# Kernel optimization log

Measured on AMD Instinct MI355X. Metric: run time of the kernel, lower is better.

The kernel has to match this reference:

```python
import jax, jax.numpy as jnp
import numpy as np
import math

B, N, D, H = 2, 64, 256, 8
DK = D // H


def setup_inputs() -> dict:
    key = jax.random.key(0)
    ks = jax.random.split(key, 12)
    s = 1.0 / math.sqrt(D)
    inp = {
        "state": jax.random.normal(ks[0], (B, N, N, D), dtype=jnp.float32),
        "mask": jnp.zeros((B, N, N, N), dtype=bool),
        "W_lk": jax.random.normal(ks[1], (D, D), dtype=jnp.float32) * s,
        "b_lk": jnp.zeros((D,), dtype=jnp.float32),
        "W_rk": jax.random.normal(ks[2], (D, D), dtype=jnp.float32) * s,
        "b_rk": jnp.zeros((D,), dtype=jnp.float32),
        "W_lv": jax.random.normal(ks[3], (D, D), dtype=jnp.float32) * s,
        "b_lv": jnp.zeros((D,), dtype=jnp.float32),
        "W_rv": jax.random.normal(ks[4], (D, D), dtype=jnp.float32) * s,
        "b_rv": jnp.zeros((D,), dtype=jnp.float32),
        "W_o": jax.random.normal(ks[5], (D, D), dtype=jnp.float32) * s,
        "b_o": jnp.zeros((D,), dtype=jnp.float32),
    }
    return inp


def _proj(x, W, b):
    # torch nn.Linear: x @ W.T + b, then view to heads
    y = jnp.einsum('bxyd,ed->bxye', x, W) + b
    return y.reshape(B, N, N, H, DK)


def reference(state, mask, W_lk, b_lk, W_rk, b_rk, W_lv, b_lv, W_rv, b_rv, W_o, b_o):
    left_k = _proj(state, W_lk, b_lk)   # [B,N,N,H,DK]
    right_k = _proj(state, W_rk, b_rk)
    left_v = _proj(state, W_lv, b_lv)
    right_v = _proj(state, W_rv, b_rv)

    # triangle-style scores over node triples (x, a, y): [B,N,N,N,H]
    scores = jnp.einsum('bxahd,bayhd->bxayh', left_k, right_k) / math.sqrt(DK)
    scores = jnp.where(mask[..., None], jnp.float32(-1000.0), scores)
    att = jax.nn.softmax(scores, axis=2)  # softmax over intermediate node a

    # val[b,x,a,y,h,d] = left_v[b,x,a,h,d] * right_v[b,a,y,h,d] (materialized as in torch)
    val = jnp.einsum('bxahd,bayhd->bxayhd', left_v, right_v)
    x = jnp.einsum('bxayh,bxayhd->bxyhd', att, val)  # sum over a
    x = x.reshape(B, N, N, D)
    return jnp.einsum('bxyd,ed->bxye', x, W_o) + b_o
```

## Files before the change

kernel.cpp:

```cpp
#include <hip/hip_runtime.h>

#define B 2
#define N 64
#define D 256
#define H 8
#define DK 32
#define M (B * N * N)

typedef __attribute__((ext_vector_type(8))) short bf16x8;
typedef __attribute__((ext_vector_type(4))) float f32x4;
typedef __attribute__((ext_vector_type(2))) float f32x2;

#define PROJ_ELEMS (2097152)

__device__ __forceinline__ ushort f2b(float f) {
    union { float f; unsigned u; } v; v.f = f;
    unsigned r = v.u + 0x7fffu + ((v.u >> 16) & 1u);
    return (ushort)(r >> 16);
}
__device__ __forceinline__ float b2f(ushort u) {
    union { unsigned u; float f; } v; v.u = ((unsigned)u) << 16; return v.f;
}
__device__ __forceinline__ f32x2 up2(unsigned u) {
    union { unsigned u; float f; } lo, hi;
    lo.u = u << 16; hi.u = u & 0xffff0000u;
    f32x2 r; r.x = lo.f; r.y = hi.f; return r;
}

__device__ __forceinline__ void glds16(const ushort* g, ushort* l) {
    __builtin_amdgcn_global_load_lds(
        (const __attribute__((address_space(1))) unsigned int*)g,
        (__attribute__((address_space(3))) unsigned int*)l, 16, 0, 0);
}

__global__ __launch_bounds__(256) void cast_all(const float* __restrict__ state,
                                                const float* __restrict__ W_lk, const float* __restrict__ W_rk,
                                                const float* __restrict__ W_lv, const float* __restrict__ W_rv,
                                                const float* __restrict__ W_o,
                                                const float* __restrict__ b_lk, const float* __restrict__ b_rk,
                                                const float* __restrict__ b_lv, const float* __restrict__ b_rv,
                                                const float* __restrict__ b_o,
                                                ushort* __restrict__ state_bf,
                                                ushort* __restrict__ Wcat,
                                                float* __restrict__ bias_cat) {
    const int gid = blockIdx.x * 256 + threadIdx.x;
    const float* Ws[5] = {W_lk, W_rk, W_lv, W_rv, W_o};
    const float* bs[5] = {b_lk, b_rk, b_lv, b_rv, b_o};

    if (gid < 1280) bias_cat[gid] = bs[gid >> 8][gid & 255];

    if (gid < 524288) {
        float4 v = *(const float4*)&state[(size_t)gid * 4];
        ushort4 o = {f2b(v.x), f2b(v.y), f2b(v.z), f2b(v.w)};
        *(ushort4*)&state_bf[(size_t)gid * 4] = o;
    } else {
        int u = gid - 524288;
        int row = u >> 6;
        int k4 = (u & 63) * 4;
        const float* W = Ws[row >> 8];
        float4 v = *(const float4*)&W[(size_t)(row & 255) * 256 + k4];
        ushort4 o = {f2b(v.x), f2b(v.y), f2b(v.z), f2b(v.w)};
        *(ushort4*)&Wcat[(size_t)row * 256 + k4] = o;
    }
}

template <int BF16OUT, int RELAYOUT>
__global__ __launch_bounds__(256) void gemm_mfma(const ushort* __restrict__ A,
                                                 const ushort* __restrict__ Bw,
                                                 const float* __restrict__ bias,
                                                 void* __restrict__ Cv, int ldc) {
    __shared__ __align__(16) ushort As[4][128 * 32];
    __shared__ __align__(16) ushort Bs[4][128 * 32];
    const int tid = threadIdx.x;
    const int lane = tid & 63;
    const int wave = tid >> 6;
    const int wm = (wave & 1) * 64;
    const int wn = (wave >> 1) * 64;
    const int row0 = blockIdx.x * 128;
    const int col0 = blockIdx.y * 128;

    const int lr = lane >> 2;
    const int lkq = (lane & 3) * 8;

    const ushort* gA0 = A + (size_t)(row0 + wave * 32 + lr) * 256 + lkq;
    const ushort* gA1 = gA0 + 16 * 256;
    const ushort* gB0 = Bw + (size_t)(col0 + wave * 32 + lr) * 256 + lkq;
    const ushort* gB1 = gB0 + 16 * 256;

    const int fr = lane & 15;
    const int fk = (lane >> 4) * 8;

    f32x4 acc[4][4] = {};

    for (int half = 0; half < 2; ++half) {
        const int k0 = half * 128;
        __syncthreads();
#pragma unroll
        for (int pp = 0; pp < 4; ++pp) {
            glds16(gA0 + k0 + pp * 32, &As[pp][(wave * 32) * 32]);
            glds16(gA1 + k0 + pp * 32, &As[pp][(wave * 32 + 16) * 32]);
            glds16(gB0 + k0 + pp * 32, &Bs[pp][(wave * 32) * 32]);
            glds16(gB1 + k0 + pp * 32, &Bs[pp][(wave * 32 + 16) * 32]);
        }
        __syncthreads();

#pragma unroll
        for (int pp = 0; pp < 4; ++pp) {
            bf16x8 af[4], bf[4];
#pragma unroll
            for (int i = 0; i < 4; ++i)
                af[i] = *(const bf16x8*)&As[pp][(wm + i * 16 + fr) * 32 + fk];
#pragma unroll
            for (int j = 0; j < 4; ++j)
                bf[j] = *(const bf16x8*)&Bs[pp][(wn + j * 16 + fr) * 32 + fk];
#pragma unroll
            for (int i = 0; i < 4; ++i)
#pragma unroll
                for (int j = 0; j < 4; ++j)
                    acc[i][j] = __builtin_amdgcn_mfma_f32_16x16x32_bf16(af[i], bf[j], acc[i][j], 0, 0, 0);
        }
    }

#pragma unroll
    for (int j = 0; j < 4; ++j) {
        const int col = col0 + wn + j * 16 + (lane & 15);
        const float bv = bias[col];
#pragma unroll
        for (int i = 0; i < 4; ++i) {
            const int rbase = row0 + wm + i * 16 + (lane >> 4) * 4;
#pragma unroll
            for (int r = 0; r < 4; ++r) {
                float o = acc[i][j][r] + bv;
                if (RELAYOUT) {
                    const int row = rbase + r;
                    const int bb = row >> 12, rr = row & 4095;
                    const int proj = col >> 8, hh = (col >> 5) & 7, dk = col & 31;
                    ((ushort*)Cv)[(size_t)proj * PROJ_ELEMS +
                                  ((size_t)(bb * 8 + hh) * 4096 + rr) * 32 + dk] = f2b(o);
                } else if (BF16OUT) {
                    ((ushort*)Cv)[(size_t)(rbase + r) * ldc + col] = f2b(o);
                } else {
                    ((float*)Cv)[(size_t)(rbase + r) * ldc + col] = o;
                }
            }
        }
    }
}

__global__ __launch_bounds__(512, 2) void fused_attn(const ushort* __restrict__ P,
                                                     const unsigned char* __restrict__ mask,
                                                     ushort* __restrict__ xbuf) {
    __shared__ __align__(16) ushort LVb[16 * 1024];
    __shared__ __align__(16) ushort RVb[32 * 512];
    __shared__ __align__(16) float atts[32 * 16 * 20];
    __shared__ float mstate[16 * 20];
    __shared__ float lstate[16 * 20];
    __shared__ float alphas[16 * 20];

    const int bh = blockIdx.z;
    const int b = bh >> 3, h = bh & 7;
    const int x0 = blockIdx.x * 16, y0 = blockIdx.y * 16;
    const int tid = threadIdx.x;
    const int lane = tid & 63, wave = tid >> 6;

    const size_t HB = (size_t)bh * 4096 * 32;
    const ushort* PLK = P + HB;
    const ushort* PRK = P + (size_t)1 * PROJ_ELEMS + HB;
    const ushort* PLV = P + (size_t)2 * PROJ_ELEMS + HB;
    const ushort* PRV = P + (size_t)3 * PROJ_ELEMS + HB;

    const int gy = lane >> 2;
    const int du = lane & 3;
    const int sx = tid >> 4, sy = tid & 15;
    if (tid < 256) {
        mstate[sx * 20 + sy] = -3.0e38f;
        lstate[sx * 20 + sy] = 0.0f;
    }

    const int sa = lane >> 2, soct = lane & 3;
    const int r2 = wave * 2;
    const int a4 = wave * 4;

    f32x2 acc[2][4] = {};
    float lacc_unused = 0.0f; (void)lacc_unused;
    const float scale = 0.17677669529663687f;

    for (int c = 0; c < 2; ++c) {
        const int ac = c * 32;
        __syncthreads();

        glds16(PLV + ((size_t)(x0 + r2) * 64 + ac + sa) * 32 + soct * 8,
               &LVb[r2 * 1024]);
        glds16(PLV + ((size_t)(x0 + r2) * 64 + ac + 16 + sa) * 32 + soct * 8,
               &LVb[r2 * 1024 + 512]);
        glds16(PLV + ((size_t)(x0 + r2 + 1) * 64 + ac + sa) * 32 + soct * 8,
               &LVb[(r2 + 1) * 1024]);
        glds16(PLV + ((size_t)(x0 + r2 + 1) * 64 + ac + 16 + sa) * 32 + soct * 8,
               &LVb[(r2 + 1) * 1024 + 512]);
#pragma unroll
        for (int k = 0; k < 4; ++k)
            glds16(PRV + ((size_t)(ac + a4 + k) * 64 + y0 + sa) * 32 + soct * 8,
                   &RVb[(a4 + k) * 512]);

        {
            const int fr = lane & 15, fk = (lane >> 4) * 8;
            const int yq = lane & 15, xq = (lane >> 4) * 4;
#pragma unroll
            for (int aw = 0; aw < 4; ++aw) {
                const int a = wave * 4 + aw;
                bf16x8 af = *(const bf16x8*)&PLK[((size_t)(x0 + fr) * 64 + ac + a) * 32 + fk];
                bf16x8 bf = *(const bf16x8*)&PRK[((size_t)(ac + a) * 64 + y0 + fr) * 32 + fk];
                f32x4 s = {};
                s = __builtin_amdgcn_mfma_f32_16x16x32_bf16(af, bf, s, 0, 0, 0);
#pragma unroll
                for (int rr = 0; rr < 4; ++rr) {
                    const int x = xq + rr;
                    float sv = s[rr] * scale;
                    if (mask[((size_t)(b * N + x0 + x) * N + ac + a) * N + y0 + yq]) sv = -1000.0f;
                    atts[(a * 16 + x) * 20 + yq] = sv;
                }
            }
        }
        __syncthreads();

        if (tid < 256) {
            float mc = -3.0e38f;
#pragma unroll
            for (int a = 0; a < 32; ++a) mc = fmaxf(mc, atts[(a * 16 + sx) * 20 + sy]);
            const float mold = mstate[sx * 20 + sy];
            const float mnew = fmaxf(mold, mc);
            const float alpha = __expf(mold - mnew);
            float ps = 0.0f;
#pragma unroll
            for (int a = 0; a < 32; ++a) {
                float p = __expf(atts[(a * 16 + sx) * 20 + sy] - mnew);
                atts[(a * 16 + sx) * 20 + sy] = p;
                ps += p;
            }
            lstate[sx * 20 + sy] = lstate[sx * 20 + sy] * alpha + ps;
            mstate[sx * 20 + sy] = mnew;
            alphas[sx * 20 + sy] = alpha;
        }
        __syncthreads();

#pragma unroll
        for (int i = 0; i < 2; ++i) {
            const float av = alphas[(wave * 2 + i) * 20 + gy];
#pragma unroll
            for (int q = 0; q < 4; ++q) acc[i][q] *= av;
        }

        {
            const unsigned* LV32 = (const unsigned*)LVb;
            const unsigned* RV32 = (const unsigned*)RVb;
#pragma unroll
            for (int a = 0; a < 32; ++a) {
                const uint4 rvw = *(const uint4*)&RV32[a * 256 + gy * 16 + du * 4];
                const f32x2 rv0 = up2(rvw.x), rv1 = up2(rvw.y);
                const f32x2 rv2 = up2(rvw.z), rv3 = up2(rvw.w);
#pragma unroll
                for (int i = 0; i < 2; ++i) {
                    const int x = wave * 2 + i;
                    const uint4 lvw = *(const uint4*)&LV32[x * 512 + a * 16 + du * 4];
                    const float w = atts[(a * 16 + x) * 20 + gy];
                    acc[i][0] += (up2(lvw.x) * w) * rv0;
                    acc[i][1] += (up2(lvw.y) * w) * rv1;
                    acc[i][2] += (up2(lvw.z) * w) * rv2;
                    acc[i][3] += (up2(lvw.w) * w) * rv3;
                }
            }
        }
    }

#pragma unroll
    for (int i = 0; i < 2; ++i) {
        const int x = wave * 2 + i;
        const float il = 1.0f / lstate[x * 20 + gy];
        ushort o[8] __attribute__((aligned(16)));
#pragma unroll
        for (int q = 0; q < 4; ++q) {
            o[2 * q]     = f2b(acc[i][q].x * il);
            o[2 * q + 1] = f2b(acc[i][q].y * il);
        }
        *(uint4*)&xbuf[(((size_t)b * N + x0 + x) * N + y0 + gy) * D + h * DK + du * 8] =
            *(const uint4*)o;
    }
}

extern "C" void kernel_launch(void* const* d_in, const int* in_sizes, int n_in,
                              void* d_out, int out_size, void* d_ws, size_t ws_size,
                              hipStream_t stream) {
    const float* state = (const float*)d_in[0];
    const unsigned char* mask = (const unsigned char*)d_in[1];
    const float* W_lk = (const float*)d_in[2];
    const float* b_lk = (const float*)d_in[3];
    const float* W_rk = (const float*)d_in[4];
    const float* b_rk = (const float*)d_in[5];
    const float* W_lv = (const float*)d_in[6];
    const float* b_lv = (const float*)d_in[7];
    const float* W_rv = (const float*)d_in[8];
    const float* b_rv = (const float*)d_in[9];
    const float* W_o = (const float*)d_in[10];
    const float* b_o = (const float*)d_in[11];
    float* out = (float*)d_out;

    char* ws = (char*)d_ws;
    ushort* P_bf = (ushort*)ws;
    ws += (size_t)4 * PROJ_ELEMS * 2;
    float* bias_cat = (float*)ws;
    ws += 1280 * 4;
    ushort* state_bf = (ushort*)ws;
    ws += (size_t)M * D * 2;
    ushort* Wcat = (ushort*)ws;
    ws += (size_t)1280 * 256 * 2;
    ushort* xbuf_bf = (ushort*)ws;

    cast_all<<<2368, 256, 0, stream>>>(state, W_lk, W_rk, W_lv, W_rv, W_o,
                                       b_lk, b_rk, b_lv, b_rv, b_o,
                                       state_bf, Wcat, bias_cat);
    gemm_mfma<1, 1><<<dim3(M / 128, 8), 256, 0, stream>>>(state_bf, Wcat, bias_cat, P_bf, 1024);
    fused_attn<<<dim3(4, 4, B * H), 512, 0, stream>>>(P_bf, mask, xbuf_bf);
    gemm_mfma<0, 0><<<dim3(M / 128, 2), 256, 0, stream>>>(xbuf_bf, Wcat + 1024 * 256, bias_cat + 1024, out, 256);
}
```

Measured before the change: 120.9 us.

## Double-buffer GEMM K-loop, shrink output GEMM tile, fold softmax exp into PV loop

The GEMM kernel now walks K in four groups of 64 with double-buffered shared memory, so loads for the next group are issued before the current group's MFMAs. It is templated on BM so the output projection can use 64-row tiles and launch twice as many blocks. In the attention kernel the separate exp/normalize pass over the scores is removed: each wave computes exp(s - m) inline while accumulating P·V and keeps its row sum in registers. The aim is to overlap load latency with compute and cut a shared-memory pass, at the cost of redundant exp work across lanes that share an x row.

Result: slower. 124.0 us (+2.5%).

```diff
diff --git a/kernel.cpp b/kernel.cpp
--- a/kernel.cpp
+++ b/kernel.cpp
@@ -64,25 +64,27 @@
     }
 }
 
-template <int BF16OUT, int RELAYOUT>
+template <int BF16OUT, int RELAYOUT, int BM>
 __global__ __launch_bounds__(256) void gemm_mfma(const ushort* __restrict__ A,
                                                  const ushort* __restrict__ Bw,
                                                  const float* __restrict__ bias,
                                                  void* __restrict__ Cv, int ldc) {
-    __shared__ __align__(16) ushort As[4][128 * 32];
-    __shared__ __align__(16) ushort Bs[4][128 * 32];
+    constexpr int IR = BM / 32;
+    __shared__ __align__(16) ushort As[2][2][BM * 32];
+    __shared__ __align__(16) ushort Bs[2][2][128 * 32];
     const int tid = threadIdx.x;
     const int lane = tid & 63;
     const int wave = tid >> 6;
-    const int wm = (wave & 1) * 64;
+    const int wm = (wave & 1) * (BM / 2);
     const int wn = (wave >> 1) * 64;
-    const int row0 = blockIdx.x * 128;
+    const int row0 = blockIdx.x * BM;
     const int col0 = blockIdx.y * 128;
 
     const int lr = lane >> 2;
     const int lkq = (lane & 3) * 8;
 
-    const ushort* gA0 = A + (size_t)(row0 + wave * 32 + lr) * 256 + lkq;
+    const int arow = (BM == 128) ? (wave * 32) : (wave * 16);
+    const ushort* gA0 = A + (size_t)(row0 + arow + lr) * 256 + lkq;
     const ushort* gA1 = gA0 + 16 * 256;
     const ushort* gB0 = Bw + (size_t)(col0 + wave * 32 + lr) * 256 + lkq;
     const ushort* gB1 = gB0 + 16 * 256;
@@ -90,35 +92,42 @@
     const int fr = lane & 15;
     const int fk = (lane >> 4) * 8;
 
-    f32x4 acc[4][4] = {};
-
-    for (int half = 0; half < 2; ++half) {
-        const int k0 = half * 128;
-        __syncthreads();
-#pragma unroll
-        for (int pp = 0; pp < 4; ++pp) {
-            glds16(gA0 + k0 + pp * 32, &As[pp][(wave * 32) * 32]);
-            glds16(gA1 + k0 + pp * 32, &As[pp][(wave * 32 + 16) * 32]);
-            glds16(gB0 + k0 + pp * 32, &Bs[pp][(wave * 32) * 32]);
-            glds16(gB1 + k0 + pp * 32, &Bs[pp][(wave * 32 + 16) * 32]);
-        }
-        __syncthreads();
-
-#pragma unroll
-        for (int pp = 0; pp < 4; ++pp) {
-            bf16x8 af[4], bf[4];
-#pragma unroll
-            for (int i = 0; i < 4; ++i)
-                af[i] = *(const bf16x8*)&As[pp][(wm + i * 16 + fr) * 32 + fk];
+    f32x4 acc[IR][4] = {};
+
+    auto stage2 = [&](int grp) {
+        const int buf = grp & 1;
+#pragma unroll
+        for (int p = 0; p < 2; ++p) {
+            const int ko = (grp * 2 + p) * 32;
+            glds16(gA0 + ko, &As[buf][p][arow * 32]);
+            if (BM == 128) glds16(gA1 + ko, &As[buf][p][(arow + 16) * 32]);
+            glds16(gB0 + ko, &Bs[buf][p][(wave * 32) * 32]);
+            glds16(gB1 + ko, &Bs[buf][p][(wave * 32 + 16) * 32]);
+        }
+    };
+
+    stage2(0);
+    __syncthreads();
+
+    for (int it = 0; it < 4; ++it) {
+        if (it < 3) stage2(it + 1);
+        const int buf = it & 1;
+#pragma unroll
+        for (int p = 0; p < 2; ++p) {
+            bf16x8 af[IR], bf[4];
+#pragma unroll
+            for (int i = 0; i < IR; ++i)
+                af[i] = *(const bf16x8*)&As[buf][p][(wm + i * 16 + fr) * 32 + fk];
 #pragma unroll
             for (int j = 0; j < 4; ++j)
-                bf[j] = *(const bf16x8*)&Bs[pp][(wn + j * 16 + fr) * 32 + fk];
-#pragma unroll
-            for (int i = 0; i < 4; ++i)
+                bf[j] = *(const bf16x8*)&Bs[buf][p][(wn + j * 16 + fr) * 32 + fk];
+#pragma unroll
+            for (int i = 0; i < IR; ++i)
 #pragma unroll
                 for (int j = 0; j < 4; ++j)
                     acc[i][j] = __builtin_amdgcn_mfma_f32_16x16x32_bf16(af[i], bf[j], acc[i][j], 0, 0, 0);
         }
+        __syncthreads();
     }
 
 #pragma unroll
@@ -126,7 +135,7 @@
         const int col = col0 + wn + j * 16 + (lane & 15);
         const float bv = bias[col];
 #pragma unroll
-        for (int i = 0; i < 4; ++i) {
+        for (int i = 0; i < IR; ++i) {
             const int rbase = row0 + wm + i * 16 + (lane >> 4) * 4;
 #pragma unroll
             for (int r = 0; r < 4; ++r) {
@@ -154,7 +163,6 @@
     __shared__ __align__(16) ushort RVb[32 * 512];
     __shared__ __align__(16) float atts[32 * 16 * 20];
     __shared__ float mstate[16 * 20];
-    __shared__ float lstate[16 * 20];
     __shared__ float alphas[16 * 20];
 
     const int bh = blockIdx.z;
@@ -172,17 +180,14 @@
     const int gy = lane >> 2;
     const int du = lane & 3;
     const int sx = tid >> 4, sy = tid & 15;
-    if (tid < 256) {
-        mstate[sx * 20 + sy] = -3.0e38f;
-        lstate[sx * 20 + sy] = 0.0f;
-    }
+    if (tid < 256) mstate[sx * 20 + sy] = -3.0e38f;
 
     const int sa = lane >> 2, soct = lane & 3;
     const int r2 = wave * 2;
     const int a4 = wave * 4;
 
     f32x2 acc[2][4] = {};
-    float lacc_unused = 0.0f; (void)lacc_unused;
+    float lacc[2] = {0.0f, 0.0f};
     const float scale = 0.17677669529663687f;
 
     for (int c = 0; c < 2; ++c) {
@@ -229,23 +234,18 @@
             for (int a = 0; a < 32; ++a) mc = fmaxf(mc, atts[(a * 16 + sx) * 20 + sy]);
             const float mold = mstate[sx * 20 + sy];
             const float mnew = fmaxf(mold, mc);
-            const float alpha = __expf(mold - mnew);
-            float ps = 0.0f;
-#pragma unroll
-            for (int a = 0; a < 32; ++a) {
-                float p = __expf(atts[(a * 16 + sx) * 20 + sy] - mnew);
-                atts[(a * 16 + sx) * 20 + sy] = p;
-                ps += p;
-            }
-            lstate[sx * 20 + sy] = lstate[sx * 20 + sy] * alpha + ps;
             mstate[sx * 20 + sy] = mnew;
-            alphas[sx * 20 + sy] = alpha;
+            alphas[sx * 20 + sy] = __expf(mold - mnew);
         }
         __syncthreads();
 
+        float mn[2];
 #pragma unroll
         for (int i = 0; i < 2; ++i) {
-            const float av = alphas[(wave * 2 + i) * 20 + gy];
+            const int x = wave * 2 + i;
+            const float av = alphas[x * 20 + gy];
+            mn[i] = mstate[x * 20 + gy];
+            lacc[i] *= av;
 #pragma unroll
             for (int q = 0; q < 4; ++q) acc[i][q] *= av;
         }
@@ -262,7 +262,9 @@
                 for (int i = 0; i < 2; ++i) {
                     const int x = wave * 2 + i;
                     const uint4 lvw = *(const uint4*)&LV32[x * 512 + a * 16 + du * 4];
-                    const float w = atts[(a * 16 + x) * 20 + gy];
+                    const float sv = atts[(a * 16 + x) * 20 + gy];
+                    const float w = __expf(sv - mn[i]);
+                    lacc[i] += w;
                     acc[i][0] += (up2(lvw.x) * w) * rv0;
                     acc[i][1] += (up2(lvw.y) * w) * rv1;
                     acc[i][2] += (up2(lvw.z) * w) * rv2;
@@ -275,7 +277,7 @@
 #pragma unroll
     for (int i = 0; i < 2; ++i) {
         const int x = wave * 2 + i;
-        const float il = 1.0f / lstate[x * 20 + gy];
+        const float il = 1.0f / lacc[i];
         ushort o[8] __attribute__((aligned(16)));
 #pragma unroll
         for (int q = 0; q < 4; ++q) {
@@ -318,7 +320,7 @@
     cast_all<<<2368, 256, 0, stream>>>(state, W_lk, W_rk, W_lv, W_rv, W_o,
                                        b_lk, b_rk, b_lv, b_rv, b_o,
                                        state_bf, Wcat, bias_cat);
-    gemm_mfma<1, 1><<<dim3(M / 128, 8), 256, 0, stream>>>(state_bf, Wcat, bias_cat, P_bf, 1024);
+    gemm_mfma<1, 1, 128><<<dim3(M / 128, 8), 256, 0, stream>>>(state_bf, Wcat, bias_cat, P_bf, 1024);
     fused_attn<<<dim3(4, 4, B * H), 512, 0, stream>>>(P_bf, mask, xbuf_bf);
-    gemm_mfma<0, 0><<<dim3(M / 128, 2), 256, 0, stream>>>(xbuf_bf, Wcat + 1024 * 256, bias_cat + 1024, out, 256);
-}
+    gemm_mfma<0, 0, 64><<<dim3(M / 64, 2), 256, 0, stream>>>(xbuf_bf, Wcat + 1024 * 256, bias_cat + 1024, out, 256);
+}
```
